# Performance work log

Hardware: AMD Instinct MI355X
Metric: run time of the kernel (lower is better)

## Reference

```python
import jax, jax.numpy as jnp
import numpy as np
from jax import lax

N = 5000
C = 81  # num_classes including background at index 0
BG_OFFSET = 1


def _iou_matrix(b):
    # b: [N,4] as x1,y1,x2,y2 -> pairwise IoU [N,N]
    x1, y1, x2, y2 = b[:, 0], b[:, 1], b[:, 2], b[:, 3]
    area = (x2 - x1) * (y2 - y1)  # [N]
    ix1 = jnp.maximum(x1[:, None], x1[None, :])
    iy1 = jnp.maximum(y1[:, None], y1[None, :])
    ix2 = jnp.minimum(x2[:, None], x2[None, :])
    iy2 = jnp.minimum(y2[:, None], y2[None, :])
    iw = jnp.maximum(ix2 - ix1, 0.0)
    ih = jnp.maximum(iy2 - iy1, 0.0)
    inter = iw * ih
    return inter / (area[:, None] + area[None, :] - inter)


def setup_inputs() -> dict:
    key = jax.random.key(0)
    k1, k2, k3 = jax.random.split(key, 3)
    # valid boxes: x1<x2, y1<y2 on a ~1024px canvas, size ~up to 256px
    xy1 = jax.random.uniform(k1, (N, 2), dtype=jnp.float32) * 1024.0
    wh = jax.random.uniform(k2, (N, 2), dtype=jnp.float32) * 256.0 + 1.0
    bboxes = jnp.concatenate([xy1, xy1 + wh], axis=1)  # [N,4]
    scores = jax.random.uniform(k3, (N, C), dtype=jnp.float32)  # [N,C]
    return {
        "bboxes": bboxes,
        "scores": scores,
        "conf_thresh": 0.6,
        "nms_thresh": 0.5,
        "max_instances": 300,
    }


def _multiclass_nms(bboxes, scores, conf_thresh, nms_thresh, max_instances):
    n = bboxes.shape[0]
    neg_inf = jnp.finfo(scores.dtype).min
    iou = _iou_matrix(bboxes)  # [N,N]

    def nms_one_class(score_c):  # score_c: [N]
        valid = score_c > conf_thresh
        masked = jnp.where(valid, score_c, neg_inf)
        order = jnp.argsort(masked)[::-1]  # descending score

        def step(suppressed, idx):
            keep = valid[idx] & ~suppressed[idx]
            new_sup = jnp.where(keep, suppressed | (iou[idx] > nms_thresh), suppressed)
            return new_sup, keep

        _, keeps = lax.scan(step, jnp.zeros((n,), bool), order)
        # scatter keep flags back to original box order
        return jnp.zeros((n,), bool).at[order].set(keeps)

    fg_scores = scores[:, BG_OFFSET:].T  # [C-1, N]
    keep = jax.vmap(nms_one_class)(fg_scores)  # [C-1, N]

    # global top-k over all (class, box) kept detections, sorted by score desc
    flat = jnp.where(keep, fg_scores, neg_inf).reshape(-1)  # [(C-1)*N]
    top_scores, top_idx = lax.top_k(flat, max_instances)
    cls = top_idx // n + BG_OFFSET  # [K]
    box = top_idx % n  # [K]
    valid_out = top_scores > neg_inf / 2

    sel_score = scores[box, cls]  # differentiable gather
    preds = jnp.concatenate([bboxes[box], sel_score[:, None]], axis=1)  # [K,5]
    preds = jnp.where(valid_out[:, None], preds, 0.0)
    labels = jnp.where(valid_out, cls, -1)
    return preds, labels


def reference(bboxes, scores, conf_thresh, nms_thresh, max_instances):
    return _multiclass_nms(bboxes, scores, conf_thresh, nms_thresh, max_instances)
```

## Files before the change

### kernel.cpp

```cpp
#include <hip/hip_runtime.h>

typedef unsigned long long u64;
typedef unsigned int u32;
typedef unsigned short u16;

#define MSORT 4096
#define TPB1  512
#define TPBF  1024
#define BOXCAP 3648
#define KCAP  3072
#define RSLOT_W 10
#define KPC   300
#define SELCAP 1024
#define PREFR 64

#define WG_SCOPE __HIP_MEMORY_SCOPE_WORKGROUP

__device__ __forceinline__ float boxArea(float4 b) {
    return __fmul_rn(__fsub_rn(b.z, b.x), __fsub_rn(b.w, b.y));
}

template<bool GE>
__device__ __forceinline__ bool iou_gt(float4 a, float area_a, float4 b, float area_b, double B) {
    float ix1 = fmaxf(a.x, b.x), iy1 = fmaxf(a.y, b.y);
    float ix2 = fminf(a.z, b.z), iy2 = fminf(a.w, b.w);
    float iw  = fmaxf(__fsub_rn(ix2, ix1), 0.0f);
    float ih  = fmaxf(__fsub_rn(iy2, iy1), 0.0f);
    float inter = __fmul_rn(iw, ih);
    float uni   = __fsub_rn(__fadd_rn(area_a, area_b), inter);
    return GE ? ((double)inter >= B * (double)uni) : ((double)inter > B * (double)uni);
}

__device__ __forceinline__ int scoreBin(u32 bits) {
    int b = (int)(bits >> 12) - 0x3F000;
    return b < 0 ? 0 : (b > 2047 ? 2047 : b);
}

template<bool GE>
__device__ __forceinline__ int prefix_nms_w0(
    const float* __restrict__ bboxes, const u64* __restrict__ sorted,
    int R, double B, int tid, int c, int N, u64* __restrict__ gkept_c)
{
    u64 key = (tid < R) ? sorted[tid] : 0;
    float4 bx = make_float4(0.f, 0.f, 0.f, 0.f);
    if (tid < R) bx = ((const float4*)bboxes)[(u32)key];
    float ar = boxArea(bx);
    u64 supB = (R >= 64) ? 0ull : (~0ull << R);
    int nk = 0;
    int i = -1;
    for (;;) {
        u64 mask = (i >= 63) ? 0ull : (~0ull << (i + 1));
        u64 alive = ~supB & mask;
        if (!alive) break;
        i = (int)__builtin_ctzll(alive);
        float4 bi;
        bi.x = __shfl(bx.x, i, 64); bi.y = __shfl(bx.y, i, 64);
        bi.z = __shfl(bx.z, i, 64); bi.w = __shfl(bx.w, i, 64);
        float ai = boxArea(bi);
        if (tid == 0) {
            u64 ki = sorted[i];
            u32 flat = (u32)c * (u32)N + (u32)ki;
            gkept_c[nk] = (ki & 0xFFFFFFFF00000000ull) | (u32)(~flat);
        }
        nk++;
        bool sup = (tid > i) && iou_gt<GE>(bi, ai, bx, ar, B);
        supB |= __ballot(sup);
    }
    return nk;
}

__global__ __launch_bounds__(TPB1, 1) void nms_select_kernel(
    const float* __restrict__ bboxes, const float* __restrict__ scores,
    const float* __restrict__ conf_ptr, const float* __restrict__ nms_ptr,
    int N, int C, int Mout, u64* __restrict__ gkept,
    u32* __restrict__ gK, u32* __restrict__ g65, u32* __restrict__ gPre,
    u32* __restrict__ gCtl, u32* __restrict__ gTick)
{
    __shared__ u64 keys[KCAP];
    __shared__ u32 hist[2048];
    __shared__ u64 keybuf[256];
    __shared__ u64 sorted[66];
    __shared__ int chunk[64];
    __shared__ int cntS, ncollS, bstarS, nkS, lastS;
    __shared__ u32 thetaS;

    const int tid = threadIdx.x;
    const int c   = blockIdx.x;
    const int nc  = gridDim.x;
    const int cls = c + 1;
    const float conf = *conf_ptr;
    const float nmsT = *nms_ptr;
    const int lane = tid & 63;

    for (int b = tid; b < 2048; b += TPB1) hist[b] = 0;
    if (tid < 66) sorted[tid] = 0;
    if (tid == 0) { cntS = 0; nkS = 0; }
    __syncthreads();

    for (int i = tid; i < N; i += TPB1) {
        float s = scores[(size_t)i * C + cls];
        bool valid = s > conf;
        u64 mask = __ballot((int)valid);
        if (valid) {
            int cntw = (int)__popcll(mask);
            int leader = (int)__builtin_ctzll(mask);
            int base = 0;
            if (lane == leader) base = atomicAdd(&cntS, cntw);
            base = __shfl(base, leader, 64);
            int off = base + (int)__popcll(mask & ((1ull << lane) - 1ull));
            if (off < KCAP) keys[off] = ((u64)__float_as_uint(s) << 32) | (u32)i;
            atomicAdd(&hist[scoreBin(__float_as_uint(s))], 1u);
        }
    }
    __syncthreads();
    const int K = cntS;
    const bool preOv = (K > KCAP);
    const int target = K < (PREFR + 1) ? K : (PREFR + 1);

    if (tid < 64) {
        int s = 0;
        #pragma unroll
        for (int b = 0; b < 32; b++) s += (int)hist[tid * 32 + b];
        chunk[tid] = s;
    }
    __syncthreads();
    if (tid == 0) {
        int acc = 0, ch = 63;
        for (; ch >= 0; ch--) { if (acc + chunk[ch] >= target) break; acc += chunk[ch]; }
        int bs = 0;
        if (ch >= 0) {
            int b = (ch << 5) + 31;
            for (; b >= (ch << 5); b--) { acc += (int)hist[b]; if (acc >= target) break; }
            bs = (b < (ch << 5)) ? (ch << 5) : b;
        }
        bstarS = bs; ncollS = 0;
    }
    __syncthreads();
    const u32 tbits = (bstarS == 0) ? 0u : (((u32)bstarS + 0x3F000u) << 12);

    const int KL = K < KCAP ? K : KCAP;
    for (int p = tid; p < KL; p += TPB1) {
        u64 k = keys[p];
        if ((u32)(k >> 32) >= tbits) {
            int pos = atomicAdd(&ncollS, 1);
            if (pos < 256) keybuf[pos] = k;
        }
    }
    __syncthreads();
    const int ncoll = ncollS;
    const bool pre = preOv || (ncoll > 256);
    for (int p = ncoll + tid; p < 256; p += TPB1) keybuf[p] = 0;
    __syncthreads();

    u64* gkept_c = gkept + (size_t)c * KPC;
    if (!pre) {
        if (tid < 256) {
            u64 my = keybuf[tid];
            int rank = 0;
            for (int j = 0; j < 256; j++) rank += (keybuf[j] > my);
            if (my && rank < PREFR + 1) sorted[rank] = my;
        }
        __syncthreads();
        const u32 tb = __float_as_uint(nmsT);
        const float Tn = __uint_as_float(tb + 1u);
        const double B = ((double)nmsT + (double)Tn) * 0.5;
        const bool geCmp = (((tb + 1u) & 1u) == 0u);
        if (tid < 64) {
            int R = ncoll < PREFR ? ncoll : PREFR;
            int nk = geCmp ? prefix_nms_w0<true >(bboxes, sorted, R, B, tid, c, N, gkept_c)
                           : prefix_nms_w0<false>(bboxes, sorted, R, B, tid, c, N, gkept_c);
            if (tid == 0) nkS = nk;
        }
        __syncthreads();
        for (int p = nkS + tid; p < KPC; p += TPB1) gkept_c[p] = 0;
    } else {
        for (int p = tid; p < KPC; p += TPB1) gkept_c[p] = 0;
    }
    if (tid == 0) {
        gK[c]   = (u32)K;
        g65[c]  = pre ? 0xFFFFFFFFu : ((ncoll >= PREFR + 1) ? (u32)(sorted[PREFR] >> 32) : 0u);
        gPre[c] = pre ? 1u : 0u;
    }
    __syncthreads();

    if (tid == 0) {
        __threadfence();
        u32 old = atomicAdd(gTick, 1u);
        lastS = (old == (u32)(nc - 1)) ? 1 : 0;
    }
    __syncthreads();
    if (!lastS) return;
    __threadfence();

    for (int b = tid; b < 2048; b += TPB1) hist[b] = 0;
    __syncthreads();
    const int total = nc * KPC;
    for (int t = tid; t < total; t += TPB1) {
        u64 k = gkept[t];
        if (k) atomicAdd(&hist[scoreBin((u32)(k >> 32))], 1u);
    }
    __syncthreads();
    if (tid < 64) {
        int s = 0;
        #pragma unroll
        for (int b = 0; b < 32; b++) s += (int)hist[tid * 32 + b];
        chunk[tid] = s;
    }
    __syncthreads();
    if (tid == 0) {
        int tot = 0;
        for (int ch = 0; ch < 64; ch++) tot += chunk[ch];
        u32 theta = 0u;
        if (tot >= Mout) {
            int acc = 0, ch = 63;
            for (; ch >= 0; ch--) { if (acc + chunk[ch] >= Mout) break; acc += chunk[ch]; }
            int b = (ch << 5) + 31;
            for (; b >= (ch << 5); b--) { acc += (int)hist[b]; if (acc >= Mout) break; }
            int bs = (b < (ch << 5)) ? (ch << 5) : b;
            theta = (bs <= 0) ? 0u : (((u32)bs + 0x3F000u) << 12);
        }
        gCtl[0] = theta;
        thetaS  = theta;
    }
    __syncthreads();
    const u32 theta = thetaS;
    for (int c2 = tid; c2 < nc; c2 += TPB1) {
        u32 need = gPre[c2];
        if (gK[c2] > PREFR && g65[c2] >= theta) need = 1u;
        gCtl[1 + c2] = need;
    }
}

template<bool GE>
__device__ __forceinline__ u64 sweep_own(
    float4 bi, float area_i, const float4 (&breg)[RSLOT_W],
    const float (&areaj)[RSLOT_W], const float4* __restrict__ boxesLds,
    int base, int nslots, int lane, double B)
{
    u64 ns = 0;
    #pragma unroll
    for (int t = 0; t < RSLOT_W; t++)
        ns |= ((u64)iou_gt<GE>(bi, area_i, breg[t], areaj[t], B)) << (base + t);
    for (int t = RSLOT_W; t < nslots; t++) {
        float4 bj = boxesLds[((base + t) << 6) | lane];
        ns |= ((u64)iou_gt<GE>(bi, area_i, bj, boxArea(bj), B)) << (base + t);
    }
    return ns;
}

template<bool GE>
__device__ __forceinline__ int greedy_full(
    const float4* __restrict__ boxesLds, u16* __restrict__ keptR,
    float4* __restrict__ pubBox, u32* __restrict__ ctl,
    const u32* __restrict__ gsi_c, const float* __restrict__ scores,
    int cls, int C, u32 thetaBits,
    int K, int smax, double B, int lane, int wave)
{
    const int SW   = (smax + 3) >> 2;
    const int base = (wave * SW < smax) ? wave * SW : smax;
    const int end  = (base + SW < smax) ? base + SW : smax;
    const int nslots = end - base;

    float4 breg[RSLOT_W];
    float  areaj[RSLOT_W];
    #pragma unroll
    for (int t = 0; t < RSLOT_W; t++) {
        float4 b = boxesLds[((base + t) << 6) | lane];
        breg[t] = b;
        areaj[t] = boxArea(b);
    }

    u64 sup;
    {
        int t = (lane < K) ? ((K - lane + 63) >> 6) : 0;
        sup = (t >= 64) ? 0ull : (~0ull << t);
    }

    u32 seen = 0;
    if (wave != 0) {
        for (;;) {
            u32 d  = __hip_atomic_load(&ctl[2], __ATOMIC_ACQUIRE, WG_SCOPE);
            u32 cn = __hip_atomic_load(&ctl[0], __ATOMIC_ACQUIRE, WG_SCOPE);
            bool prog = (seen < cn);
            while (seen < cn) {
                float4 bi = pubBox[seen]; seen++;
                sup |= sweep_own<GE>(bi, boxArea(bi), breg, areaj, boxesLds, base, nslots, lane, B);
            }
            if (d) return -1;
            u32 aw = __hip_atomic_load(&ctl[1], __ATOMIC_ACQUIRE, WG_SCOPE);
            if (aw == (u32)wave) {
                u32 cn2 = __hip_atomic_load(&ctl[0], __ATOMIC_ACQUIRE, WG_SCOPE);
                while (seen < cn2) {
                    float4 bi = pubBox[seen]; seen++;
                    sup |= sweep_own<GE>(bi, boxArea(bi), breg, areaj, boxesLds, base, nslots, lane, B);
                }
                break;
            }
            if (!prog) __builtin_amdgcn_s_sleep(1);
        }
    }

    u32 nk = seen;
    const u32 seen0 = seen;
    int scur = base - 1;
    float4 bcur = make_float4(0.f, 0.f, 0.f, 0.f);
    float  acur = 0.f;
    int js = base << 6;

    for (;;) {
        int s = js >> 6;
        while (s > scur) {
            scur++;
            if (scur < end) {
                bcur = boxesLds[(scur << 6) | lane];
                acur = boxArea(bcur);
                u64 bit = 0;
                for (u32 k = seen0; k < nk; k++) {
                    float4 bk = pubBox[k];
                    bit |= ((u64)iou_gt<GE>(bk, boxArea(bk), bcur, acur, B));
                }
                sup |= bit << scur;
            }
        }
        if (scur >= end) {
            if (wave == 3) {
                if (lane == 0) __hip_atomic_store(&ctl[2], 1u, __ATOMIC_RELEASE, WG_SCOPE);
                return (int)nk;
            }
            if (lane == 0) __hip_atomic_store(&ctl[1], (u32)(wave + 1), __ATOMIC_RELEASE, WG_SCOPE);
            return -1;
        }
        u64 bal = __ballot((int)(((~sup) >> scur) & 1ull)) & (~0ull << (js & 63));
        if (bal == 0) { js = (scur + 1) << 6; continue; }
        int i = (scur << 6) + (int)__builtin_ctzll(bal);

        if (thetaBits) {
            u32 idx = gsi_c[i];
            float sc = scores[(size_t)idx * C + cls];
            if (__float_as_uint(sc) < thetaBits) {
                if (lane == 0) __hip_atomic_store(&ctl[2], 1u, __ATOMIC_RELEASE, WG_SCOPE);
                return (int)nk;
            }
        }
        float4 bi = boxesLds[i];
        if (lane == 0) { pubBox[nk] = bi; keptR[nk] = (u16)i; }
        nk++;
        if (nk >= KPC) {
            if (lane == 0) {
                __hip_atomic_store(&ctl[0], nk, __ATOMIC_RELEASE, WG_SCOPE);
                __hip_atomic_store(&ctl[2], 1u, __ATOMIC_RELEASE, WG_SCOPE);
            }
            return (int)nk;
        }
        if (lane == 0) __hip_atomic_store(&ctl[0], nk, __ATOMIC_RELEASE, WG_SCOPE);
        sup |= ((u64)iou_gt<GE>(bi, boxArea(bi), bcur, acur, B)) << scur;
        js = i + 1;
    }
}

__global__ __launch_bounds__(TPBF, 1) void nms_full_kernel(
    const float* __restrict__ bboxes, const float* __restrict__ scores,
    const float* __restrict__ conf_ptr, const float* __restrict__ nms_ptr,
    int N, int C, int Mout, const u32* __restrict__ gCtl,
    u32* __restrict__ gsi, u64* __restrict__ gkept,
    u32* __restrict__ gTick, float* __restrict__ out)
{
    __shared__ __align__(16) char smem[63856];
    __shared__ int cntS, lastS, selCount, bstar2S;

    const int tid = threadIdx.x;
    const int c   = blockIdx.x;
    const int nc  = gridDim.x;
    const int cls = c + 1;

    if (gCtl[1 + c] != 0u) {
        u64*    sortbuf  = (u64*)smem;
        float4* boxesLds = (float4*)smem;
        u16*    keptR    = (u16*)(smem + 58368);
        u32*    ctl      = (u32*)(smem + 58976);
        float4* pubBox   = (float4*)(smem + 58992);
        const float conf = *conf_ptr;
        const float nmsT = *nms_ptr;
        const u32 thetaBits = gCtl[0];

        if (tid == 0) cntS = 0;
        __syncthreads();
        for (int i = tid; i < N; i += TPBF) {
            float s = scores[(size_t)i * C + cls];
            if (s > conf) {
                int p = atomicAdd(&cntS, 1);
                if (p < MSORT) sortbuf[p] = ((u64)__float_as_uint(s) << 32) | (u32)i;
            }
        }
        __syncthreads();
        int K = cntS; if (K > BOXCAP) K = BOXCAP;
        int M = 64; while (M < K) M <<= 1;
        for (int p = K + tid; p < M; p += TPBF) sortbuf[p] = 0;
        __syncthreads();
        for (int kk = 2; kk <= M; kk <<= 1) {
            for (int j = kk >> 1; j > 0; j >>= 1) {
                for (int i = tid; i < M; i += TPBF) {
                    int ixj = i ^ j;
                    if (ixj > i) {
                        u64 a = sortbuf[i], b = sortbuf[ixj];
                        if (((i & kk) == 0) ? (a < b) : (a > b)) { sortbuf[i] = b; sortbuf[ixj] = a; }
                    }
                }
                __syncthreads();
            }
        }
        u32 myIdx[MSORT / TPBF];
        #pragma unroll
        for (int t = 0; t < MSORT / TPBF; t++) myIdx[t] = (u32)sortbuf[t * TPBF + tid];
        __syncthreads();
        u32* gsi_c = gsi + (size_t)c * BOXCAP;
        #pragma unroll
        for (int t = 0; t < MSORT / TPBF; t++) {
            int r = t * TPBF + tid;
            if (r < K) {
                u32 idx = myIdx[t];
                gsi_c[r] = idx;
                boxesLds[r] = ((const float4*)bboxes)[idx];
            }
        }
        if (tid == 0) { ctl[0] = 0; ctl[1] = 0; ctl[2] = 0; }
        __syncthreads();

        if (tid < 256) {
            const int lane = tid & 63;
            const int wave = tid >> 6;
            const u32 tb = __float_as_uint(nmsT);
            const float Tn = __uint_as_float(tb + 1u);
            const double B = ((double)nmsT + (double)Tn) * 0.5;
            const bool geCmp = (((tb + 1u) & 1u) == 0u);
            const int smax = (K + 63) >> 6;
            int ret = geCmp ? greedy_full<true >(boxesLds, keptR, pubBox, ctl, gsi_c, scores, cls, C, thetaBits, K, smax, B, lane, wave)
                            : greedy_full<false>(boxesLds, keptR, pubBox, ctl, gsi_c, scores, cls, C, thetaBits, K, smax, B, lane, wave);
            if (ret >= 0) {
                int kept = ret; if (kept > KPC) kept = KPC;
                u64* gkept_c = gkept + (size_t)c * KPC;
                for (int p = lane; p < kept; p += 64) {
                    int rank = keptR[p];
                    u32 idx = gsi_c[rank];
                    float sc = scores[(size_t)idx * C + cls];
                    u32 flat = (u32)c * (u32)N + idx;
                    gkept_c[p] = ((u64)__float_as_uint(sc) << 32) | (u32)(~flat);
                }
                for (int p = kept + lane; p < KPC; p += 64) gkept_c[p] = 0;
            }
        }
    }
    __syncthreads();

    if (tid == 0) {
        __threadfence();
        u32 old = atomicAdd(gTick, 1u);
        lastS = (old == (u32)(nc - 1)) ? 1 : 0;
    }
    __syncthreads();
    if (!lastS) return;
    __threadfence();

    u32* hist  = (u32*)smem;
    int* chunk = (int*)(smem + 8192);
    u64* sel   = (u64*)(smem + 8448);

    const int total = nc * KPC;
    for (int b = tid; b < 2048; b += TPBF) hist[b] = 0;
    if (tid == 0) selCount = 0;
    __syncthreads();
    for (int t = tid; t < total; t += TPBF) {
        u64 k = gkept[t];
        if (k) atomicAdd(&hist[scoreBin((u32)(k >> 32))], 1u);
    }
    __syncthreads();
    if (tid < 64) {
        int s = 0;
        #pragma unroll
        for (int b = 0; b < 32; b++) s += (int)hist[tid * 32 + b];
        chunk[tid] = s;
    }
    __syncthreads();
    if (tid == 0) {
        int acc = 0, ch = 63;
        for (; ch >= 0; ch--) { if (acc + chunk[ch] >= Mout) break; acc += chunk[ch]; }
        int bs = 0;
        if (ch >= 0) {
            int b = (ch << 5) + 31;
            for (; b >= (ch << 5); b--) { acc += (int)hist[b]; if (acc >= Mout) break; }
            bs = (b < (ch << 5)) ? (ch << 5) : b;
        }
        bstar2S = bs;
    }
    __syncthreads();
    const int bstar = bstar2S;
    for (int t = tid; t < total; t += TPBF) {
        u64 k = gkept[t];
        if (k && scoreBin((u32)(k >> 32)) >= bstar) {
            int p = atomicAdd(&selCount, 1);
            if (p < SELCAP) sel[p] = k;
        }
    }
    __syncthreads();
    int cnt = selCount; if (cnt > SELCAP) cnt = SELCAP;
    int SM = 512; while (SM < cnt) SM <<= 1;
    for (int p = cnt + tid; p < SM; p += TPBF) sel[p] = 0;
    __syncthreads();
    for (int kk = 2; kk <= SM; kk <<= 1) {
        for (int j = kk >> 1; j > 0; j >>= 1) {
            for (int i = tid; i < SM; i += TPBF) {
                int ixj = i ^ j;
                if (ixj > i) {
                    u64 a = sel[i], b = sel[ixj];
                    if (((i & kk) == 0) ? (a < b) : (a > b)) { sel[i] = b; sel[ixj] = a; }
                }
            }
            __syncthreads();
        }
    }

    for (int t = tid; t < Mout; t += TPBF) {
        u64 k = (t < SM) ? sel[t] : 0;
        float px1 = 0.f, py1 = 0.f, px2 = 0.f, py2 = 0.f, ps = 0.f, plab = -1.0f;
        if (k) {
            float s  = __uint_as_float((u32)(k >> 32));
            u32 flat = ~((u32)k);
            int cc   = (int)(flat / (u32)N);
            int box  = (int)(flat - (u32)cc * (u32)N);
            float4 bb = ((const float4*)bboxes)[box];
            px1 = bb.x; py1 = bb.y; px2 = bb.z; py2 = bb.w; ps = s;
            plab = (float)(cc + 1);
        }
        out[t * 5 + 0] = px1;
        out[t * 5 + 1] = py1;
        out[t * 5 + 2] = px2;
        out[t * 5 + 3] = py2;
        out[t * 5 + 4] = ps;
        out[Mout * 5 + t] = plab;
    }
}

extern "C" void kernel_launch(void* const* d_in, const int* in_sizes, int n_in,
                              void* d_out, int out_size, void* d_ws, size_t ws_size,
                              hipStream_t stream) {
    const float* bboxes = (const float*)d_in[0];
    const float* scores = (const float*)d_in[1];
    const float* conf   = (const float*)d_in[2];
    const float* nmsT   = (const float*)d_in[3];

    const int N    = in_sizes[0] / 4;
    const int C    = in_sizes[1] / N;
    const int nc   = C - 1;
    const int Mout = out_size / 6;

    char* wsb = (char*)d_ws;
    size_t off = 0;
    u32* gsi   = (u32*)(wsb + off); off += (size_t)nc * BOXCAP * sizeof(u32);
    u64* gkept = (u64*)(wsb + off); off += (size_t)nc * KPC * sizeof(u64);
    u32* gK    = (u32*)(wsb + off); off += (size_t)((nc + 1) & ~1) * sizeof(u32);
    u32* g65   = (u32*)(wsb + off); off += (size_t)((nc + 1) & ~1) * sizeof(u32);
    u32* gPre  = (u32*)(wsb + off); off += (size_t)((nc + 1) & ~1) * sizeof(u32);
    u32* gCtl  = (u32*)(wsb + off); off += (size_t)((nc + 2) & ~1) * sizeof(u32);
    u32* gTick = (u32*)(wsb + off);

    hipMemsetAsync(gTick, 0, 2 * sizeof(u32), stream);
    nms_select_kernel<<<nc, TPB1, 0, stream>>>(bboxes, scores, conf, nmsT, N, C, Mout,
                                               gkept, gK, g65, gPre, gCtl, gTick);
    nms_full_kernel<<<nc, TPBF, 0, stream>>>(bboxes, scores, conf, nmsT, N, C, Mout,
                                             gCtl, gsi, gkept, gTick + 1, (float*)d_out);
}
```

Before: 134.2 us.

## Add coalesced scatter pass to bucket candidates per class before NMS

```diff
diff --git a/kernel.cpp b/kernel.cpp
--- a/kernel.cpp
+++ b/kernel.cpp
@@ -5,14 +5,13 @@
 typedef unsigned short u16;
 
 #define MSORT 4096
-#define TPB1  512
 #define TPBF  1024
 #define BOXCAP 3648
-#define KCAP  3072
 #define RSLOT_W 10
 #define KPC   300
 #define SELCAP 1024
 #define PREFR 64
+#define CMAX  256
 
 #define WG_SCOPE __HIP_MEMORY_SCOPE_WORKGROUP
 
@@ -34,6 +33,46 @@
 __device__ __forceinline__ int scoreBin(u32 bits) {
     int b = (int)(bits >> 12) - 0x3F000;
     return b < 0 ? 0 : (b > 2047 ? 2047 : b);
+}
+
+__global__ __launch_bounds__(256, 1) void nms_scatter_kernel(
+    const float* __restrict__ scores, const float* __restrict__ conf_ptr,
+    int N, int C, int rpb, u32* __restrict__ gCnt, u64* __restrict__ gCand)
+{
+    __shared__ int cnt[CMAX];
+    __shared__ int base[CMAX];
+    const int tid = threadIdx.x;
+    const int r0 = blockIdx.x * rpb;
+    if (r0 >= N) return;
+    const int r1 = (r0 + rpb < N) ? r0 + rpb : N;
+    const int nel = (r1 - r0) * C;
+    const float* sp = scores + (size_t)r0 * C;
+    const float conf = *conf_ptr;
+
+    for (int i = tid; i < C; i += 256) cnt[i] = 0;
+    __syncthreads();
+    for (int f = tid; f < nel; f += 256) {
+        float s = sp[f];
+        int cls = f % C;
+        if (cls > 0 && s > conf) atomicAdd(&cnt[cls], 1);
+    }
+    __syncthreads();
+    for (int i = tid; i < C; i += 256) {
+        int n = cnt[i];
+        base[i] = (i > 0 && n > 0) ? (int)atomicAdd(&gCnt[i], (u32)n) : 0;
+        cnt[i] = 0;
+    }
+    __syncthreads();
+    for (int f = tid; f < nel; f += 256) {
+        float s = sp[f];
+        int cls = f % C;
+        if (cls > 0 && s > conf) {
+            int off = atomicAdd(&cnt[cls], 1);
+            int i = r0 + f / C;
+            gCand[(size_t)(cls - 1) * N + base[cls] + off] =
+                ((u64)__float_as_uint(s) << 32) | (u32)i;
+        }
+    }
 }
 
 template<bool GE>
@@ -69,52 +108,34 @@
     return nk;
 }
 
-__global__ __launch_bounds__(TPB1, 1) void nms_select_kernel(
-    const float* __restrict__ bboxes, const float* __restrict__ scores,
-    const float* __restrict__ conf_ptr, const float* __restrict__ nms_ptr,
-    int N, int C, int Mout, u64* __restrict__ gkept,
-    u32* __restrict__ gK, u32* __restrict__ g65, u32* __restrict__ gPre,
+__global__ __launch_bounds__(TPBF, 1) void nms_select_kernel(
+    const float* __restrict__ bboxes, const float* __restrict__ nms_ptr,
+    int N, int Mout, const u64* __restrict__ gCand, const u32* __restrict__ gCnt,
+    u64* __restrict__ gkept, u32* __restrict__ g65, u32* __restrict__ gPre,
     u32* __restrict__ gCtl, u32* __restrict__ gTick)
 {
-    __shared__ u64 keys[KCAP];
     __shared__ u32 hist[2048];
     __shared__ u64 keybuf[256];
     __shared__ u64 sorted[66];
     __shared__ int chunk[64];
-    __shared__ int cntS, ncollS, bstarS, nkS, lastS;
+    __shared__ int ncollS, bstarS, nkS, lastS;
     __shared__ u32 thetaS;
 
     const int tid = threadIdx.x;
     const int c   = blockIdx.x;
     const int nc  = gridDim.x;
-    const int cls = c + 1;
-    const float conf = *conf_ptr;
     const float nmsT = *nms_ptr;
-    const int lane = tid & 63;
-
-    for (int b = tid; b < 2048; b += TPB1) hist[b] = 0;
+    const int K = (int)gCnt[c + 1];
+    const u64* cand = gCand + (size_t)c * N;
+
+    for (int b = tid; b < 2048; b += TPBF) hist[b] = 0;
     if (tid < 66) sorted[tid] = 0;
-    if (tid == 0) { cntS = 0; nkS = 0; }
-    __syncthreads();
-
-    for (int i = tid; i < N; i += TPB1) {
-        float s = scores[(size_t)i * C + cls];
-        bool valid = s > conf;
-        u64 mask = __ballot((int)valid);
-        if (valid) {
-            int cntw = (int)__popcll(mask);
-            int leader = (int)__builtin_ctzll(mask);
-            int base = 0;
-            if (lane == leader) base = atomicAdd(&cntS, cntw);
-            base = __shfl(base, leader, 64);
-            int off = base + (int)__popcll(mask & ((1ull << lane) - 1ull));
-            if (off < KCAP) keys[off] = ((u64)__float_as_uint(s) << 32) | (u32)i;
-            atomicAdd(&hist[scoreBin(__float_as_uint(s))], 1u);
-        }
-    }
-    __syncthreads();
-    const int K = cntS;
-    const bool preOv = (K > KCAP);
+    if (tid == 0) { ncollS = 0; nkS = 0; }
+    __syncthreads();
+
+    for (int t = tid; t < K; t += TPBF)
+        atomicAdd(&hist[scoreBin((u32)(cand[t] >> 32))], 1u);
+    __syncthreads();
     const int target = K < (PREFR + 1) ? K : (PREFR + 1);
 
     if (tid < 64) {
@@ -133,14 +154,13 @@
             for (; b >= (ch << 5); b--) { acc += (int)hist[b]; if (acc >= target) break; }
             bs = (b < (ch << 5)) ? (ch << 5) : b;
         }
-        bstarS = bs; ncollS = 0;
+        bstarS = bs;
     }
     __syncthreads();
     const u32 tbits = (bstarS == 0) ? 0u : (((u32)bstarS + 0x3F000u) << 12);
 
-    const int KL = K < KCAP ? K : KCAP;
-    for (int p = tid; p < KL; p += TPB1) {
-        u64 k = keys[p];
+    for (int t = tid; t < K; t += TPBF) {
+        u64 k = cand[t];
         if ((u32)(k >> 32) >= tbits) {
             int pos = atomicAdd(&ncollS, 1);
             if (pos < 256) keybuf[pos] = k;
@@ -148,8 +168,8 @@
     }
     __syncthreads();
     const int ncoll = ncollS;
-    const bool pre = preOv || (ncoll > 256);
-    for (int p = ncoll + tid; p < 256; p += TPB1) keybuf[p] = 0;
+    const bool pre = (ncoll > 256);
+    for (int p = ncoll + tid; p < 256; p += TPBF) keybuf[p] = 0;
     __syncthreads();
 
     u64* gkept_c = gkept + (size_t)c * KPC;
@@ -172,12 +192,11 @@
             if (tid == 0) nkS = nk;
         }
         __syncthreads();
-        for (int p = nkS + tid; p < KPC; p += TPB1) gkept_c[p] = 0;
+        for (int p = nkS + tid; p < KPC; p += TPBF) gkept_c[p] = 0;
     } else {
-        for (int p = tid; p < KPC; p += TPB1) gkept_c[p] = 0;
+        for (int p = tid; p < KPC; p += TPBF) gkept_c[p] = 0;
     }
     if (tid == 0) {
-        gK[c]   = (u32)K;
         g65[c]  = pre ? 0xFFFFFFFFu : ((ncoll >= PREFR + 1) ? (u32)(sorted[PREFR] >> 32) : 0u);
         gPre[c] = pre ? 1u : 0u;
     }
@@ -192,10 +211,10 @@
     if (!lastS) return;
     __threadfence();
 
-    for (int b = tid; b < 2048; b += TPB1) hist[b] = 0;
+    for (int b = tid; b < 2048; b += TPBF) hist[b] = 0;
     __syncthreads();
     const int total = nc * KPC;
-    for (int t = tid; t < total; t += TPB1) {
+    for (int t = tid; t < total; t += TPBF) {
         u64 k = gkept[t];
         if (k) atomicAdd(&hist[scoreBin((u32)(k >> 32))], 1u);
     }
@@ -224,9 +243,9 @@
     }
     __syncthreads();
     const u32 theta = thetaS;
-    for (int c2 = tid; c2 < nc; c2 += TPB1) {
+    for (int c2 = tid; c2 < nc; c2 += TPBF) {
         u32 need = gPre[c2];
-        if (gK[c2] > PREFR && g65[c2] >= theta) need = 1u;
+        if ((int)gCnt[c2 + 1] > PREFR && g65[c2] >= theta) need = 1u;
         gCtl[1 + c2] = need;
     }
 }
@@ -252,8 +271,7 @@
 __device__ __forceinline__ int greedy_full(
     const float4* __restrict__ boxesLds, u16* __restrict__ keptR,
     float4* __restrict__ pubBox, u32* __restrict__ ctl,
-    const u32* __restrict__ gsi_c, const float* __restrict__ scores,
-    int cls, int C, u32 thetaBits,
+    const u64* __restrict__ gsk_c, u32 thetaBits,
     int K, int smax, double B, int lane, int wave)
 {
     const int SW   = (smax + 3) >> 2;
@@ -334,13 +352,9 @@
         if (bal == 0) { js = (scur + 1) << 6; continue; }
         int i = (scur << 6) + (int)__builtin_ctzll(bal);
 
-        if (thetaBits) {
-            u32 idx = gsi_c[i];
-            float sc = scores[(size_t)idx * C + cls];
-            if (__float_as_uint(sc) < thetaBits) {
-                if (lane == 0) __hip_atomic_store(&ctl[2], 1u, __ATOMIC_RELEASE, WG_SCOPE);
-                return (int)nk;
-            }
+        if (thetaBits && (u32)(gsk_c[i] >> 32) < thetaBits) {
+            if (lane == 0) __hip_atomic_store(&ctl[2], 1u, __ATOMIC_RELEASE, WG_SCOPE);
+            return (int)nk;
         }
         float4 bi = boxesLds[i];
         if (lane == 0) { pubBox[nk] = bi; keptR[nk] = (u16)i; }
@@ -359,19 +373,17 @@
 }
 
 __global__ __launch_bounds__(TPBF, 1) void nms_full_kernel(
-    const float* __restrict__ bboxes, const float* __restrict__ scores,
-    const float* __restrict__ conf_ptr, const float* __restrict__ nms_ptr,
-    int N, int C, int Mout, const u32* __restrict__ gCtl,
-    u32* __restrict__ gsi, u64* __restrict__ gkept,
+    const float* __restrict__ bboxes, const float* __restrict__ nms_ptr,
+    int N, int Mout, const u64* __restrict__ gCand, const u32* __restrict__ gCnt,
+    const u32* __restrict__ gCtl, u64* __restrict__ gsk, u64* __restrict__ gkept,
     u32* __restrict__ gTick, float* __restrict__ out)
 {
     __shared__ __align__(16) char smem[63856];
-    __shared__ int cntS, lastS, selCount, bstar2S;
+    __shared__ int lastS, selCount, bstar2S;
 
     const int tid = threadIdx.x;
     const int c   = blockIdx.x;
     const int nc  = gridDim.x;
-    const int cls = c + 1;
 
     if (gCtl[1 + c] != 0u) {
         u64*    sortbuf  = (u64*)smem;
@@ -379,21 +391,13 @@
         u16*    keptR    = (u16*)(smem + 58368);
         u32*    ctl      = (u32*)(smem + 58976);
         float4* pubBox   = (float4*)(smem + 58992);
-        const float conf = *conf_ptr;
         const float nmsT = *nms_ptr;
         const u32 thetaBits = gCtl[0];
-
-        if (tid == 0) cntS = 0;
-        __syncthreads();
-        for (int i = tid; i < N; i += TPBF) {
-            float s = scores[(size_t)i * C + cls];
-            if (s > conf) {
-                int p = atomicAdd(&cntS, 1);
-                if (p < MSORT) sortbuf[p] = ((u64)__float_as_uint(s) << 32) | (u32)i;
-            }
-        }
-        __syncthreads();
-        int K = cntS; if (K > BOXCAP) K = BOXCAP;
+        const u64* cand = gCand + (size_t)c * N;
+
+        int K = (int)gCnt[c + 1];
+        if (K > MSORT) K = MSORT;
+        for (int p = tid; p < K; p += TPBF) sortbuf[p] = cand[p];
         int M = 64; while (M < K) M <<= 1;
         for (int p = K + tid; p < M; p += TPBF) sortbuf[p] = 0;
         __syncthreads();
@@ -409,18 +413,18 @@
                 __syncthreads();
             }
         }
-        u32 myIdx[MSORT / TPBF];
+        if (K > BOXCAP) K = BOXCAP;
+        u64 myKey[MSORT / TPBF];
         #pragma unroll
-        for (int t = 0; t < MSORT / TPBF; t++) myIdx[t] = (u32)sortbuf[t * TPBF + tid];
+        for (int t = 0; t < MSORT / TPBF; t++) myKey[t] = sortbuf[t * TPBF + tid];
         __syncthreads();
-        u32* gsi_c = gsi + (size_t)c * BOXCAP;
+        u64* gsk_c = gsk + (size_t)c * BOXCAP;
         #pragma unroll
         for (int t = 0; t < MSORT / TPBF; t++) {
             int r = t * TPBF + tid;
             if (r < K) {
-                u32 idx = myIdx[t];
-                gsi_c[r] = idx;
-                boxesLds[r] = ((const float4*)bboxes)[idx];
+                gsk_c[r] = myKey[t];
+                boxesLds[r] = ((const float4*)bboxes)[(u32)myKey[t]];
             }
         }
         if (tid == 0) { ctl[0] = 0; ctl[1] = 0; ctl[2] = 0; }
@@ -434,17 +438,15 @@
             const double B = ((double)nmsT + (double)Tn) * 0.5;
             const bool geCmp = (((tb + 1u) & 1u) == 0u);
             const int smax = (K + 63) >> 6;
-            int ret = geCmp ? greedy_full<true >(boxesLds, keptR, pubBox, ctl, gsi_c, scores, cls, C, thetaBits, K, smax, B, lane, wave)
-                            : greedy_full<false>(boxesLds, keptR, pubBox, ctl, gsi_c, scores, cls, C, thetaBits, K, smax, B, lane, wave);
+            int ret = geCmp ? greedy_full<true >(boxesLds, keptR, pubBox, ctl, gsk_c, thetaBits, K, smax, B, lane, wave)
+                            : greedy_full<false>(boxesLds, keptR, pubBox, ctl, gsk_c, thetaBits, K, smax, B, lane, wave);
             if (ret >= 0) {
                 int kept = ret; if (kept > KPC) kept = KPC;
                 u64* gkept_c = gkept + (size_t)c * KPC;
                 for (int p = lane; p < kept; p += 64) {
-                    int rank = keptR[p];
-                    u32 idx = gsi_c[rank];
-                    float sc = scores[(size_t)idx * C + cls];
-                    u32 flat = (u32)c * (u32)N + idx;
-                    gkept_c[p] = ((u64)__float_as_uint(sc) << 32) | (u32)(~flat);
+                    u64 key = gsk_c[keptR[p]];
+                    u32 flat = (u32)c * (u32)N + (u32)key;
+                    gkept_c[p] = (key & 0xFFFFFFFF00000000ull) | (u32)(~flat);
                 }
                 for (int p = kept + lane; p < KPC; p += 64) gkept_c[p] = 0;
             }
@@ -555,17 +557,21 @@
 
     char* wsb = (char*)d_ws;
     size_t off = 0;
-    u32* gsi   = (u32*)(wsb + off); off += (size_t)nc * BOXCAP * sizeof(u32);
+    u64* gCand = (u64*)(wsb + off); off += (size_t)nc * N * sizeof(u64);
+    u64* gsk   = (u64*)(wsb + off); off += (size_t)nc * BOXCAP * sizeof(u64);
     u64* gkept = (u64*)(wsb + off); off += (size_t)nc * KPC * sizeof(u64);
-    u32* gK    = (u32*)(wsb + off); off += (size_t)((nc + 1) & ~1) * sizeof(u32);
     u32* g65   = (u32*)(wsb + off); off += (size_t)((nc + 1) & ~1) * sizeof(u32);
     u32* gPre  = (u32*)(wsb + off); off += (size_t)((nc + 1) & ~1) * sizeof(u32);
     u32* gCtl  = (u32*)(wsb + off); off += (size_t)((nc + 2) & ~1) * sizeof(u32);
-    u32* gTick = (u32*)(wsb + off);
-
-    hipMemsetAsync(gTick, 0, 2 * sizeof(u32), stream);
-    nms_select_kernel<<<nc, TPB1, 0, stream>>>(bboxes, scores, conf, nmsT, N, C, Mout,
-                                               gkept, gK, g65, gPre, gCtl, gTick);
-    nms_full_kernel<<<nc, TPBF, 0, stream>>>(bboxes, scores, conf, nmsT, N, C, Mout,
-                                             gCtl, gsi, gkept, gTick + 1, (float*)d_out);
-}
+    u32* gCnt  = (u32*)(wsb + off);
+    u32* gTick = gCnt + C;
+
+    hipMemsetAsync(gCnt, 0, (C + 2) * sizeof(u32), stream);
+    const int rpb = 40;
+    const int nbA = (N + rpb - 1) / rpb;
+    nms_scatter_kernel<<<nbA, 256, 0, stream>>>(scores, conf, N, C, rpb, gCnt, gCand);
+    nms_select_kernel<<<nc, TPBF, 0, stream>>>(bboxes, nmsT, N, Mout, gCand, gCnt,
+                                               gkept, g65, gPre, gCtl, gTick);
+    nms_full_kernel<<<nc, TPBF, 0, stream>>>(bboxes, nmsT, N, Mout, gCand, gCnt,
+                                             gCtl, gsk, gkept, gTick + 1, (float*)d_out);
+}
```

New measurement: 141.6 us. 1.05x slower.
